# Performance work log

Measured on AMD Instinct MI355X. Metric: run time of the kernel, lower is better.

Reference implementation:

```python
import jax, jax.numpy as jnp
import numpy as np

H = 512
INPUT_DIM = 13
OUTPUT_DIM = 1
W_DIM = (INPUT_DIM + OUTPUT_DIM) * H  # 7168
R = 256
N = 2048
LOG_2PI = float(np.log(2.0 * np.pi))


def setup_inputs() -> dict:
    key = jax.random.key(0)
    k1, k2, k3 = jax.random.split(key, 3)
    x = jax.random.normal(k1, (N, INPUT_DIM), dtype=jnp.float32)
    y = jax.random.normal(k2, (N, OUTPUT_DIM), dtype=jnp.float32)
    w = jax.random.normal(k3, (R, W_DIM), dtype=jnp.float32)
    return {"x": x, "y": y, "w": w}


def reference(x, y, w):
    # Batched version of FFReLU.loglik: for each weight sample r,
    #   w1 = w[r, :H*13].reshape(H, 13); w2 = w[r, H*13:].reshape(1, H)
    #   mu = w2 @ relu(w1 @ x.T)            -> [1, N]
    #   logprob[r] = Normal(mu.T, 1).log_prob(y).T
    w1_dim = H * INPUT_DIM
    w1 = w[:, :w1_dim].reshape(R, H, INPUT_DIM)       # [R, H, 13]
    w2 = w[:, w1_dim:].reshape(R, H)                  # [R, H] (output_dim = 1)
    hidden = jax.nn.relu(jnp.einsum('rhi,ni->rnh', w1, x))  # [R, N, H]
    mu = jnp.einsum('rnh,rh->rn', hidden, w2)         # [R, N]
    resid = y[:, 0][None, :] - mu                     # [R, N]
    log_p = -0.5 * resid * resid - 0.5 * LOG_2PI      # Normal(mu, 1) log-prob
    return log_p
```

## Files before the change

### kernel.cpp

```cpp
#include <hip/hip_runtime.h>

#define HH 512
#define IND 13
#define NN 2048
#define RR 256
#define WDIM 7168
#define W1DIM 6656
#define XTILE 256
#define NTHREADS 256
#define NEG_HALF_LOG_2PI (-0.91893853320467274f)

typedef __attribute__((ext_vector_type(8))) short short8;
typedef __attribute__((ext_vector_type(4))) float f32x4;
typedef __attribute__((ext_vector_type(2))) float f32x2;

__device__ __forceinline__ short f2bf(float f) {
    unsigned u = __float_as_uint(f);
    u += 0x7fffu + ((u >> 16) & 1u);
    return (short)(u >> 16);
}
__device__ __forceinline__ float bf2f(short s) {
    return __uint_as_float(((unsigned)(unsigned short)s) << 16);
}

__global__ __launch_bounds__(NTHREADS, 3)
void ffrelu_mfma_kernel(const float* __restrict__ x,
                        const float* __restrict__ y,
                        const float* __restrict__ w,
                        float* __restrict__ out) {
    __shared__ short Als[HH * 16];
    __shared__ float w2s[HH];

    const int tid = threadIdx.x;
    const int r = blockIdx.x;
    const int wave = tid >> 6;
    const int lane = tid & 63;
    const int m = lane & 15;
    const int q = lane >> 4;

    const float* wr = w + (size_t)r * WDIM;

    {
        int* Ai = (int*)Als;
        for (int g = tid; g < HH * 8; g += NTHREADS) Ai[g] = 0;
    }
    __syncthreads();
    for (int g = tid; g < W1DIM; g += NTHREADS) {
        int h = g / IND;
        int i = g - h * IND;
        Als[h * 16 + i] = f2bf(wr[g]);
    }
    for (int g = tid; g < HH; g += NTHREADS) w2s[g] = wr[W1DIM + g];
    __syncthreads();

    const int nb = blockIdx.y * XTILE + wave * 64;
    const bool lo  = (q >= 2);
    const bool hi8 = (q & 1);
    short8 bfrag[4];
#pragma unroll
    for (int nt = 0; nt < 4; ++nt) {
        const float* xp = x + (size_t)(nb + nt * 16 + m) * IND;
        short hs[13], ls[13];
#pragma unroll
        for (int i = 0; i < 13; ++i) {
            float v = xp[i];
            hs[i] = f2bf(v);
            ls[i] = f2bf(v - bf2f(hs[i]));
        }
        short s[13];
#pragma unroll
        for (int i = 0; i < 13; ++i) s[i] = lo ? ls[i] : hs[i];
        short8 b;
        b[0] = hi8 ? s[8]        : s[0];
        b[1] = hi8 ? s[9]        : s[1];
        b[2] = hi8 ? s[10]       : s[2];
        b[3] = hi8 ? s[11]       : s[3];
        b[4] = hi8 ? s[12]       : s[4];
        b[5] = hi8 ? (short)0    : s[5];
        b[6] = hi8 ? (short)0    : s[6];
        b[7] = hi8 ? (short)0    : s[7];
        bfrag[nt] = b;
    }

    f32x2 muv[4][2];
#pragma unroll
    for (int i = 0; i < 4; ++i) {
        muv[i][0] = (f32x2){0.0f, 0.0f};
        muv[i][1] = (f32x2){0.0f, 0.0f};
    }
    const f32x2 zero2 = {0.0f, 0.0f};

#pragma unroll 2
    for (int t = 0; t < 32; ++t) {
        const short8 a = *(const short8*)&Als[(t * 16 + m) * 16 + (q & 1) * 8];
        const f32x4 wv = *(const f32x4*)&w2s[t * 16 + q * 4];
        const f32x2 wv01 = {wv[0], wv[1]};
        const f32x2 wv23 = {wv[2], wv[3]};
#pragma unroll
        for (int nt = 0; nt < 4; ++nt) {
            f32x4 c = {0.0f, 0.0f, 0.0f, 0.0f};
            c = __builtin_amdgcn_mfma_f32_16x16x32_bf16(a, bfrag[nt], c, 0, 0, 0);
            f32x2 c01 = {c[0], c[1]};
            f32x2 c23 = {c[2], c[3]};
            c01 = __builtin_elementwise_max(c01, zero2);
            c23 = __builtin_elementwise_max(c23, zero2);
            muv[nt][0] += c01 * wv01;
            muv[nt][1] += c23 * wv23;
        }
    }

    float mu[4];
#pragma unroll
    for (int nt = 0; nt < 4; ++nt) {
        f32x2 p = muv[nt][0] + muv[nt][1];
        float v = p[0] + p[1];
        v += __shfl_xor(v, 16, 64);
        v += __shfl_xor(v, 32, 64);
        mu[nt] = v;
    }

    float mu0;
    if (q == 0)      mu0 = mu[0];
    else if (q == 1) mu0 = mu[1];
    else if (q == 2) mu0 = mu[2];
    else             mu0 = mu[3];

    const int n0 = nb + lane;
    float resid0 = y[n0] - mu0;
    out[(size_t)r * NN + n0] = fmaf(-0.5f * resid0, resid0, NEG_HALF_LOG_2PI);
}

extern "C" void kernel_launch(void* const* d_in, const int* in_sizes, int n_in,
                              void* d_out, int out_size, void* d_ws, size_t ws_size,
                              hipStream_t stream) {
    const float* x = (const float*)d_in[0];
    const float* y = (const float*)d_in[1];
    const float* w = (const float*)d_in[2];
    float* out = (float*)d_out;

    dim3 grid(RR, NN / XTILE);
    dim3 block(NTHREADS);
    ffrelu_mfma_kernel<<<grid, block, 0, stream>>>(x, y, w, out);
}
```

Baseline: 96.44 us.

## Process two N-halves per block to amortize weight staging; vectorize LDS fill

Each block now covers 512 x-rows in two passes over the same LDS-resident bf16 weight tile, halving the grid and the number of times each weight row is converted and staged. The LDS fill writes each padded 16-element row with two vector stores, which removes the separate zeroing pass and one barrier. The hi/lo split of x uses truncation instead of round-to-nearest, which is cheaper but changes the rounding of the compensated bf16 split. Fewer blocks means less parallelism across the GPU.

```diff
diff --git a/kernel.cpp b/kernel.cpp
--- a/kernel.cpp
+++ b/kernel.cpp
@@ -6,7 +6,7 @@
 #define RR 256
 #define WDIM 7168
 #define W1DIM 6656
-#define XTILE 256
+#define NBLK 512
 #define NTHREADS 256
 #define NEG_HALF_LOG_2PI (-0.91893853320467274f)
 
@@ -18,9 +18,6 @@
     unsigned u = __float_as_uint(f);
     u += 0x7fffu + ((u >> 16) & 1u);
     return (short)(u >> 16);
-}
-__device__ __forceinline__ float bf2f(short s) {
-    return __uint_as_float(((unsigned)(unsigned short)s) << 16);
 }
 
 __global__ __launch_bounds__(NTHREADS, 3)
@@ -40,94 +37,102 @@
 
     const float* wr = w + (size_t)r * WDIM;
 
-    {
-        int* Ai = (int*)Als;
-        for (int g = tid; g < HH * 8; g += NTHREADS) Ai[g] = 0;
+#pragma unroll
+    for (int rr = 0; rr < 2; ++rr) {
+        const int h = tid * 2 + rr;
+        const float* p = wr + (size_t)h * IND;
+        short tmp[16];
+#pragma unroll
+        for (int i = 0; i < 13; ++i) tmp[i] = f2bf(p[i]);
+        tmp[13] = 0; tmp[14] = 0; tmp[15] = 0;
+        *(short8*)&Als[h * 16]     = *(short8*)&tmp[0];
+        *(short8*)&Als[h * 16 + 8] = *(short8*)&tmp[8];
     }
-    __syncthreads();
-    for (int g = tid; g < W1DIM; g += NTHREADS) {
-        int h = g / IND;
-        int i = g - h * IND;
-        Als[h * 16 + i] = f2bf(wr[g]);
-    }
-    for (int g = tid; g < HH; g += NTHREADS) w2s[g] = wr[W1DIM + g];
+    w2s[tid]       = wr[W1DIM + tid];
+    w2s[tid + 256] = wr[W1DIM + tid + 256];
     __syncthreads();
 
-    const int nb = blockIdx.y * XTILE + wave * 64;
     const bool lo  = (q >= 2);
     const bool hi8 = (q & 1);
-    short8 bfrag[4];
-#pragma unroll
-    for (int nt = 0; nt < 4; ++nt) {
-        const float* xp = x + (size_t)(nb + nt * 16 + m) * IND;
-        short hs[13], ls[13];
-#pragma unroll
-        for (int i = 0; i < 13; ++i) {
-            float v = xp[i];
-            hs[i] = f2bf(v);
-            ls[i] = f2bf(v - bf2f(hs[i]));
-        }
-        short s[13];
-#pragma unroll
-        for (int i = 0; i < 13; ++i) s[i] = lo ? ls[i] : hs[i];
-        short8 b;
-        b[0] = hi8 ? s[8]        : s[0];
-        b[1] = hi8 ? s[9]        : s[1];
-        b[2] = hi8 ? s[10]       : s[2];
-        b[3] = hi8 ? s[11]       : s[3];
-        b[4] = hi8 ? s[12]       : s[4];
-        b[5] = hi8 ? (short)0    : s[5];
-        b[6] = hi8 ? (short)0    : s[6];
-        b[7] = hi8 ? (short)0    : s[7];
-        bfrag[nt] = b;
-    }
-
-    f32x2 muv[4][2];
-#pragma unroll
-    for (int i = 0; i < 4; ++i) {
-        muv[i][0] = (f32x2){0.0f, 0.0f};
-        muv[i][1] = (f32x2){0.0f, 0.0f};
-    }
     const f32x2 zero2 = {0.0f, 0.0f};
 
-#pragma unroll 2
-    for (int t = 0; t < 32; ++t) {
-        const short8 a = *(const short8*)&Als[(t * 16 + m) * 16 + (q & 1) * 8];
-        const f32x4 wv = *(const f32x4*)&w2s[t * 16 + q * 4];
-        const f32x2 wv01 = {wv[0], wv[1]};
-        const f32x2 wv23 = {wv[2], wv[3]};
+    for (int half = 0; half < 2; ++half) {
+        const int nb = blockIdx.y * NBLK + half * 256 + wave * 64;
+
+        short8 bfrag[4];
 #pragma unroll
         for (int nt = 0; nt < 4; ++nt) {
-            f32x4 c = {0.0f, 0.0f, 0.0f, 0.0f};
-            c = __builtin_amdgcn_mfma_f32_16x16x32_bf16(a, bfrag[nt], c, 0, 0, 0);
-            f32x2 c01 = {c[0], c[1]};
-            f32x2 c23 = {c[2], c[3]};
-            c01 = __builtin_elementwise_max(c01, zero2);
-            c23 = __builtin_elementwise_max(c23, zero2);
-            muv[nt][0] += c01 * wv01;
-            muv[nt][1] += c23 * wv23;
+            const float* xp = x + (size_t)(nb + nt * 16 + m) * IND;
+            short hs[13], ls[13];
+#pragma unroll
+            for (int i = 0; i < 13; ++i) {
+                float v = xp[i];
+                unsigned u = __float_as_uint(v);
+                hs[i] = (short)(u >> 16);
+                float res = v - __uint_as_float(u & 0xffff0000u);
+                ls[i] = (short)(__float_as_uint(res) >> 16);
+            }
+            short s[13];
+#pragma unroll
+            for (int i = 0; i < 13; ++i) s[i] = lo ? ls[i] : hs[i];
+            short8 b;
+            b[0] = hi8 ? s[8]     : s[0];
+            b[1] = hi8 ? s[9]     : s[1];
+            b[2] = hi8 ? s[10]    : s[2];
+            b[3] = hi8 ? s[11]    : s[3];
+            b[4] = hi8 ? s[12]    : s[4];
+            b[5] = hi8 ? (short)0 : s[5];
+            b[6] = hi8 ? (short)0 : s[6];
+            b[7] = hi8 ? (short)0 : s[7];
+            bfrag[nt] = b;
         }
+
+        f32x2 muv[4][2];
+#pragma unroll
+        for (int i = 0; i < 4; ++i) {
+            muv[i][0] = zero2;
+            muv[i][1] = zero2;
+        }
+
+#pragma unroll 2
+        for (int t = 0; t < 32; ++t) {
+            const short8 a = *(const short8*)&Als[(t * 16 + m) * 16 + (q & 1) * 8];
+            const f32x4 wv = *(const f32x4*)&w2s[t * 16 + q * 4];
+            const f32x2 wv01 = {wv[0], wv[1]};
+            const f32x2 wv23 = {wv[2], wv[3]};
+#pragma unroll
+            for (int nt = 0; nt < 4; ++nt) {
+                f32x4 c = {0.0f, 0.0f, 0.0f, 0.0f};
+                c = __builtin_amdgcn_mfma_f32_16x16x32_bf16(a, bfrag[nt], c, 0, 0, 0);
+                f32x2 c01 = {c[0], c[1]};
+                f32x2 c23 = {c[2], c[3]};
+                c01 = __builtin_elementwise_max(c01, zero2);
+                c23 = __builtin_elementwise_max(c23, zero2);
+                muv[nt][0] += c01 * wv01;
+                muv[nt][1] += c23 * wv23;
+            }
+        }
+
+        float mu[4];
+#pragma unroll
+        for (int nt = 0; nt < 4; ++nt) {
+            f32x2 p = muv[nt][0] + muv[nt][1];
+            float v = p[0] + p[1];
+            v += __shfl_xor(v, 16, 64);
+            v += __shfl_xor(v, 32, 64);
+            mu[nt] = v;
+        }
+
+        float mu0;
+        if (q == 0)      mu0 = mu[0];
+        else if (q == 1) mu0 = mu[1];
+        else if (q == 2) mu0 = mu[2];
+        else             mu0 = mu[3];
+
+        const int n0 = nb + lane;
+        float resid0 = y[n0] - mu0;
+        out[(size_t)r * NN + n0] = fmaf(-0.5f * resid0, resid0, NEG_HALF_LOG_2PI);
     }
-
-    float mu[4];
-#pragma unroll
-    for (int nt = 0; nt < 4; ++nt) {
-        f32x2 p = muv[nt][0] + muv[nt][1];
-        float v = p[0] + p[1];
-        v += __shfl_xor(v, 16, 64);
-        v += __shfl_xor(v, 32, 64);
-        mu[nt] = v;
-    }
-
-    float mu0;
-    if (q == 0)      mu0 = mu[0];
-    else if (q == 1) mu0 = mu[1];
-    else if (q == 2) mu0 = mu[2];
-    else             mu0 = mu[3];
-
-    const int n0 = nb + lane;
-    float resid0 = y[n0] - mu0;
-    out[(size_t)r * NN + n0] = fmaf(-0.5f * resid0, resid0, NEG_HALF_LOG_2PI);
 }
 
 extern "C" void kernel_launch(void* const* d_in, const int* in_sizes, int n_in,
@@ -138,7 +143,7 @@
     const float* w = (const float*)d_in[2];
     float* out = (float*)d_out;
 
-    dim3 grid(RR, NN / XTILE);
+    dim3 grid(RR, NN / NBLK);
     dim3 block(NTHREADS);
     ffrelu_mfma_kernel<<<grid, block, 0, stream>>>(x, y, w, out);
 }
```

Measured after the change: 92.59 us. 4.0% less time.
